# Kernel optimization log

Measured on AMD Instinct MI355X. Metric: run time of the kernel, lower is better.

## Reference

```python
import jax, jax.numpy as jnp
from jax import lax
import numpy as np

PAD_IDX = 4
KERNEL_SIZES = (2, 3, 4, 5)
N_FILTERS = 32
D_EMB = 8
D_OUT = 64
VOCAB = 5
B, L = 4096, 512
LN_EPS = 1e-5


def setup_inputs() -> dict:
    key = jax.random.key(0)
    ks = jax.random.split(key, 32)
    inp = {}
    inp['x_idx'] = jax.random.randint(ks[0], (B, L), 0, VOCAB, dtype=jnp.int64 if jax.config.jax_enable_x64 else jnp.int32)
    emb = jax.random.normal(ks[1], (VOCAB, D_EMB), dtype=jnp.float32) * 0.1
    inp['emb'] = emb.at[PAD_IDX].set(0.0)  # padding_idx row zero
    for i, kz in enumerate(KERNEL_SIZES):
        inp[f'conv_w{i}'] = jax.random.normal(ks[2 + 2 * i], (N_FILTERS, D_EMB, kz), dtype=jnp.float32) * (1.0 / np.sqrt(D_EMB * kz))
        inp[f'conv_b{i}'] = jnp.zeros((N_FILTERS,), jnp.float32)
        inp[f'att_w{i}'] = jax.random.normal(ks[3 + 2 * i], (N_FILTERS,), dtype=jnp.float32) * (1.0 / np.sqrt(N_FILTERS))
        inp[f'att_b{i}'] = jnp.zeros((1,), jnp.float32)
    inp['proj_w'] = jax.random.normal(ks[20], (D_OUT, N_FILTERS * len(KERNEL_SIZES)), dtype=jnp.float32) * (1.0 / np.sqrt(N_FILTERS * len(KERNEL_SIZES)))
    inp['proj_b'] = jnp.zeros((D_OUT,), jnp.float32)
    inp['gamma'] = jnp.ones((D_OUT,), jnp.float32)
    inp['beta'] = jnp.zeros((D_OUT,), jnp.float32)
    return inp


def _branch(X, W, b, aw, ab):
    # X: [B, C_in, L]; W: [C_out, C_in, ks]
    h = lax.conv_general_dilated(X, W, (1,), 'VALID',
                                 dimension_numbers=('NCH', 'OIH', 'NCH'))
    h = jax.nn.gelu(h + b[None, :, None], approximate=False)     # [B, F, L']
    scores = jnp.einsum('bfl,f->bl', h, aw) + ab[0]              # linear attn score
    w = jax.nn.softmax(scores, axis=1)                           # over positions
    return jnp.einsum('bfl,bl->bf', h, w)                        # weighted pool -> [B, F]


def reference(x_idx, emb, conv_w0, conv_b0, conv_w1, conv_b1, conv_w2, conv_b2,
              conv_w3, conv_b3, att_w0, att_b0, att_w1, att_b1, att_w2, att_b2,
              att_w3, att_b3, proj_w, proj_b, gamma, beta):
    emb = emb.at[PAD_IDX].set(0.0)
    X = emb[x_idx].transpose(0, 2, 1)  # [B, d_emb, L]
    feats = [
        _branch(X, conv_w0, conv_b0, att_w0, att_b0),
        _branch(X, conv_w1, conv_b1, att_w1, att_b1),
        _branch(X, conv_w2, conv_b2, att_w2, att_b2),
        _branch(X, conv_w3, conv_b3, att_w3, att_b3),
    ]
    z = jnp.concatenate(feats, axis=1)                 # [B, 4*F]
    z = z @ proj_w.T + proj_b                          # [B, D_OUT]
    z = jax.nn.gelu(z, approximate=False)
    mu = jnp.mean(z, axis=-1, keepdims=True)
    var = jnp.var(z, axis=-1, keepdims=True)
    return (z - mu) / jnp.sqrt(var + LN_EPS) * gamma + beta
```

## Files before the change

kernel.cpp:

```cpp
#include <hip/hip_runtime.h>
#include <math.h>

#define BATCH 4096
#define SEQL  512
#define NF    32
#define DEMB  8
#define DOUT  64

#define NWIN_TOTAL 3900
#define HWIN_OFF   4096

__device__ __forceinline__ float gelu_exact(float x) {
    return 0.5f * x * (1.0f + erff(x * 0.70710678118654752f));
}

__global__ __launch_bounds__(256) void precompute_tables(
    const float* __restrict__ emb,
    const float* __restrict__ cw0, const float* __restrict__ cb0,
    const float* __restrict__ aw0, const float* __restrict__ ab0,
    const float* __restrict__ cw1, const float* __restrict__ cb1,
    const float* __restrict__ aw1, const float* __restrict__ ab1,
    const float* __restrict__ cw2, const float* __restrict__ cb2,
    const float* __restrict__ aw2, const float* __restrict__ ab2,
    const float* __restrict__ cw3, const float* __restrict__ cb3,
    const float* __restrict__ aw3, const float* __restrict__ ab3,
    float* __restrict__ ws)
{
    const int gid = blockIdx.x * blockDim.x + threadIdx.x;
    if (gid >= NWIN_TOTAL * NF) return;
    const int wgid = gid >> 5;
    const int f    = gid & 31;

    int w, ks;
    const float *cw, *cb, *aw, *ab;
    if (wgid < 25)       { w = wgid;       ks = 2; cw = cw0; cb = cb0; aw = aw0; ab = ab0; }
    else if (wgid < 150) { w = wgid - 25;  ks = 3; cw = cw1; cb = cb1; aw = aw1; ab = ab1; }
    else if (wgid < 775) { w = wgid - 150; ks = 4; cw = cw2; cb = cb2; aw = aw2; ab = ab2; }
    else                 { w = wgid - 775; ks = 5; cw = cw3; cb = cb3; aw = aw3; ab = ab3; }

    float h = cb[f];
    int ww = w;
    for (int t = ks - 1; t >= 0; --t) {
        int d = ww % 5; ww /= 5;
        const float* e = emb + d * DEMB;
#pragma unroll
        for (int c = 0; c < DEMB; ++c)
            h += e[c] * cw[(f * DEMB + c) * ks + t];
    }
    float g = gelu_exact(h);
    ws[HWIN_OFF + wgid * NF + f] = g;

    float s = g * aw[f];
#pragma unroll
    for (int off = 16; off; off >>= 1) s += __shfl_xor(s, off, 32);
    if (f == 0) ws[wgid] = s + ab[0];
}

__global__ __launch_bounds__(256) void fused_main(
    const int*   __restrict__ xidx,
    const float* __restrict__ ws,
    const float* __restrict__ projw, const float* __restrict__ projb,
    const float* __restrict__ gamma, const float* __restrict__ beta,
    float* __restrict__ out)
{
    __shared__ int    xs[SEQL];
    __shared__ float2 pw[4][SEQL];
    __shared__ float  feat[4 * NF];

    const int b   = blockIdx.x;
    const int tid = threadIdx.x;

#pragma unroll
    for (int i = tid; i < SEQL / 4; i += 256)
        ((int4*)xs)[i] = ((const int4*)(xidx + b * SEQL))[i];
    __syncthreads();

    const int wave = tid >> 6;
    const int lane = tid & 63;

    constexpr int KS[4]  = {2, 3, 4, 5};
    constexpr int LP[4]  = {511, 510, 509, 508};
    constexpr int SWB[4] = {0, 25, 150, 775};

    const int ks = KS[wave];
    const int Lp = LP[wave];
    const float* swin = ws + SWB[wave];
    const float* hwin = ws + HWIN_OFF + SWB[wave] * NF;

    float sv[8];
    float m = -INFINITY;
#pragma unroll
    for (int it = 0; it < 8; ++it) {
        int l = lane + it * 64;
        int w = 0; float s = -INFINITY;
        if (l < Lp) {
            w = xs[l];
            for (int t = 1; t < ks; ++t) w = w * 5 + xs[l + t];
            s = swin[w];
        }
        pw[wave][l].y = __int_as_float(w * (NF * 4));
        sv[it] = s;
        m = fmaxf(m, s);
    }
#pragma unroll
    for (int off = 32; off; off >>= 1) m = fmaxf(m, __shfl_xor(m, off));

    float ssum = 0.0f;
#pragma unroll
    for (int it = 0; it < 8; ++it) {
        int l = lane + it * 64;
        float e = __expf(sv[it] - m);
        pw[wave][l].x = e;
        ssum += e;
    }
#pragma unroll
    for (int off = 32; off; off >>= 1) ssum += __shfl_xor(ssum, off);
    const float inv = 1.0f / ssum;

    const int quad = lane & 7;
    const int pg   = lane >> 3;

    float a0 = 0.f, a1 = 0.f, a2 = 0.f, a3 = 0.f;
#pragma unroll 16
    for (int it = 0; it < 64; ++it) {
        const int pos = it * 8 + pg;
        float2 t = pw[wave][pos];
        const float p = t.x;
        const char* rowp = (const char*)hwin + __float_as_int(t.y);
        float4 r = *(const float4*)(rowp + quad * 16);
        a0 += p * r.x; a1 += p * r.y; a2 += p * r.z; a3 += p * r.w;
    }

#pragma unroll
    for (int off = 8; off < 64; off <<= 1) {
        a0 += __shfl_xor(a0, off);
        a1 += __shfl_xor(a1, off);
        a2 += __shfl_xor(a2, off);
        a3 += __shfl_xor(a3, off);
    }
    if (lane < 8) {
        float* fp = feat + wave * NF + lane * 4;
        fp[0] = a0 * inv; fp[1] = a1 * inv; fp[2] = a2 * inv; fp[3] = a3 * inv;
    }
    __syncthreads();

    if (tid < DOUT) {
        float z = projb[tid];
        const float4* pwr = (const float4*)(projw + tid * (4 * NF));
#pragma unroll
        for (int q = 0; q < 32; ++q) {
            float4 wq = pwr[q];
            const float* fj = feat + q * 4;
            z += wq.x * fj[0] + wq.y * fj[1] + wq.z * fj[2] + wq.w * fj[3];
        }
        z = gelu_exact(z);

        float s1 = z, s2 = z * z;
#pragma unroll
        for (int off = 32; off; off >>= 1) {
            s1 += __shfl_xor(s1, off);
            s2 += __shfl_xor(s2, off);
        }
        const float mu  = s1 * (1.0f / 64.0f);
        const float var = s2 * (1.0f / 64.0f) - mu * mu;
        const float r   = rsqrtf(var + 1e-5f);
        out[b * DOUT + tid] = (z - mu) * r * gamma[tid] + beta[tid];
    }
}

extern "C" void kernel_launch(void* const* d_in, const int* in_sizes, int n_in,
                              void* d_out, int out_size, void* d_ws, size_t ws_size,
                              hipStream_t stream) {
    const int*   xidx = (const int*)d_in[0];
    const float* emb  = (const float*)d_in[1];
    const float* cw[4]; const float* cb[4]; const float* aw[4]; const float* ab[4];
    for (int i = 0; i < 4; ++i) {
        cw[i] = (const float*)d_in[2 + 4 * i];
        cb[i] = (const float*)d_in[3 + 4 * i];
        aw[i] = (const float*)d_in[4 + 4 * i];
        ab[i] = (const float*)d_in[5 + 4 * i];
    }
    const float* projw = (const float*)d_in[18];
    const float* projb = (const float*)d_in[19];
    const float* gm    = (const float*)d_in[20];
    const float* bt    = (const float*)d_in[21];
    float* ws  = (float*)d_ws;
    float* out = (float*)d_out;

    hipLaunchKernelGGL(precompute_tables, dim3((NWIN_TOTAL * NF + 255) / 256), dim3(256), 0, stream,
                       emb,
                       cw[0], cb[0], aw[0], ab[0],
                       cw[1], cb[1], aw[1], ab[1],
                       cw[2], cb[2], aw[2], ab[2],
                       cw[3], cb[3], aw[3], ab[3],
                       ws);

    hipLaunchKernelGGL(fused_main, dim3(BATCH), dim3(256), 0, stream,
                       xidx, ws, projw, projb, gm, bt, out);
}
```

Measured before the change: 163.2 us.

## Store window tables in fp16, stage small tables in LDS, split pooling across waves

The precomputed GELU window tables are now stored as fp16. The ks=2 and ks=3 tables are copied into shared memory per block, while the ks=4 and ks=5 tables are still read from global/L2 as half8 vectors. The pooling loop is restructured so each wave handles a quarter of the positions for all four branches, with normalized softmax weights in LDS and a cross-wave partial-sum reduction. This aims to cut gather bandwidth and improve load balance, at the cost of extra LDS, one more barrier and fp16 rounding of the conv activations.

```diff
diff --git a/kernel.cpp b/kernel.cpp
--- a/kernel.cpp
+++ b/kernel.cpp
@@ -1,5 +1,8 @@
 #include <hip/hip_runtime.h>
 #include <math.h>
+
+typedef _Float16 half_t;
+typedef _Float16 half8 __attribute__((ext_vector_type(8)));
 
 #define BATCH 4096
 #define SEQL  512
@@ -48,7 +51,7 @@
             h += e[c] * cw[(f * DEMB + c) * ks + t];
     }
     float g = gelu_exact(h);
-    ws[HWIN_OFF + wgid * NF + f] = g;
+    ((half_t*)(ws + HWIN_OFF))[wgid * NF + f] = (half_t)g;
 
     float s = g * aw[f];
 #pragma unroll
@@ -64,83 +67,115 @@
     float* __restrict__ out)
 {
     __shared__ int    xs[SEQL];
-    __shared__ float2 pw[4][SEQL];
+    __shared__ float  pwS[4][SEQL];
+    __shared__ int    poffS[4][SEQL];
+    __shared__ half_t tabS[150 * NF];
+    __shared__ float  partial[4][4][NF];
     __shared__ float  feat[4 * NF];
 
     const int b   = blockIdx.x;
     const int tid = threadIdx.x;
+    const half_t* hwin16 = (const half_t*)(ws + HWIN_OFF);
 
 #pragma unroll
     for (int i = tid; i < SEQL / 4; i += 256)
         ((int4*)xs)[i] = ((const int4*)(xidx + b * SEQL))[i];
+#pragma unroll
+    for (int i = tid; i < 600; i += 256)
+        ((float4*)tabS)[i] = ((const float4*)hwin16)[i];
     __syncthreads();
 
     const int wave = tid >> 6;
     const int lane = tid & 63;
 
     constexpr int KS[4]  = {2, 3, 4, 5};
-    constexpr int LP[4]  = {511, 510, 509, 508};
     constexpr int SWB[4] = {0, 25, 150, 775};
 
-    const int ks = KS[wave];
-    const int Lp = LP[wave];
-    const float* swin = ws + SWB[wave];
-    const float* hwin = ws + HWIN_OFF + SWB[wave] * NF;
-
-    float sv[8];
-    float m = -INFINITY;
-#pragma unroll
-    for (int it = 0; it < 8; ++it) {
-        int l = lane + it * 64;
-        int w = 0; float s = -INFINITY;
-        if (l < Lp) {
-            w = xs[l];
-            for (int t = 1; t < ks; ++t) w = w * 5 + xs[l + t];
-            s = swin[w];
-        }
-        pw[wave][l].y = __int_as_float(w * (NF * 4));
-        sv[it] = s;
-        m = fmaxf(m, s);
-    }
-#pragma unroll
-    for (int off = 32; off; off >>= 1) m = fmaxf(m, __shfl_xor(m, off));
-
-    float ssum = 0.0f;
-#pragma unroll
-    for (int it = 0; it < 8; ++it) {
-        int l = lane + it * 64;
-        float e = __expf(sv[it] - m);
-        pw[wave][l].x = e;
-        ssum += e;
-    }
-#pragma unroll
-    for (int off = 32; off; off >>= 1) ssum += __shfl_xor(ssum, off);
-    const float inv = 1.0f / ssum;
-
-    const int quad = lane & 7;
-    const int pg   = lane >> 3;
-
-    float a0 = 0.f, a1 = 0.f, a2 = 0.f, a3 = 0.f;
-#pragma unroll 16
-    for (int it = 0; it < 64; ++it) {
-        const int pos = it * 8 + pg;
-        float2 t = pw[wave][pos];
-        const float p = t.x;
-        const char* rowp = (const char*)hwin + __float_as_int(t.y);
-        float4 r = *(const float4*)(rowp + quad * 16);
-        a0 += p * r.x; a1 += p * r.y; a2 += p * r.z; a3 += p * r.w;
-    }
-
-#pragma unroll
-    for (int off = 8; off < 64; off <<= 1) {
-        a0 += __shfl_xor(a0, off);
-        a1 += __shfl_xor(a1, off);
-        a2 += __shfl_xor(a2, off);
-        a3 += __shfl_xor(a3, off);
-    }
-    if (lane < 8) {
-        float* fp = feat + wave * NF + lane * 4;
-        fp[0] = a0 * inv; fp[1] = a1 * inv; fp[2] = a2 * inv; fp[3] = a3 * inv;
+    {
+        const int ks = KS[wave];
+        const int Lp = SEQL + 1 - ks;
+        const float* swin = ws + SWB[wave];
+
+        float sv[8];
+        float m = -INFINITY;
+#pragma unroll
+        for (int it = 0; it < 8; ++it) {
+            int l = lane + it * 64;
+            int w = 0; float s = -INFINITY;
+            if (l < Lp) {
+                w = xs[l];
+                for (int t = 1; t < ks; ++t) w = w * 5 + xs[l + t];
+                s = swin[w];
+            }
+            poffS[wave][l] = w << 6;
+            sv[it] = s;
+            m = fmaxf(m, s);
+        }
+#pragma unroll
+        for (int off = 32; off; off >>= 1) m = fmaxf(m, __shfl_xor(m, off));
+
+        float ssum = 0.0f;
+#pragma unroll
+        for (int it = 0; it < 8; ++it) {
+            sv[it] = __expf(sv[it] - m);
+            ssum += sv[it];
+        }
+#pragma unroll
+        for (int off = 32; off; off >>= 1) ssum += __shfl_xor(ssum, off);
+        const float inv = 1.0f / ssum;
+#pragma unroll
+        for (int it = 0; it < 8; ++it)
+            pwS[wave][lane + it * 64] = sv[it] * inv;
+    }
+    __syncthreads();
+
+    const int pl = lane & 15;
+    const int fq = lane >> 4;
+
+    const half_t* gtab2 = hwin16 + SWB[2] * NF;
+    const half_t* gtab3 = hwin16 + SWB[3] * NF;
+
+    float acc[4][8];
+#pragma unroll
+    for (int c = 0; c < 4; ++c)
+#pragma unroll
+        for (int j = 0; j < 8; ++j) acc[c][j] = 0.0f;
+
+#pragma unroll
+    for (int c = 0; c < 4; ++c) {
+#pragma unroll
+        for (int it = 0; it < 8; ++it) {
+            const int pos = (wave << 7) + (it << 4) + pl;
+            const float p = pwS[c][pos];
+            const int  off = poffS[c][pos];
+            half8 r;
+            if (c == 0)      r = *(const half8*)((const char*)tabS + off + fq * 16);
+            else if (c == 1) r = *(const half8*)((const char*)(tabS + 25 * NF) + off + fq * 16);
+            else if (c == 2) r = *(const half8*)((const char*)gtab2 + off + fq * 16);
+            else             r = *(const half8*)((const char*)gtab3 + off + fq * 16);
+#pragma unroll
+            for (int j = 0; j < 8; ++j)
+                acc[c][j] += p * (float)r[j];
+        }
+    }
+
+#pragma unroll
+    for (int c = 0; c < 4; ++c)
+#pragma unroll
+        for (int j = 0; j < 8; ++j) {
+            float v = acc[c][j];
+            v += __shfl_xor(v, 1);
+            v += __shfl_xor(v, 2);
+            v += __shfl_xor(v, 4);
+            v += __shfl_xor(v, 8);
+            if (pl == 0) partial[wave][c][fq * 8 + j] = v;
+        }
+    __syncthreads();
+
+    if (tid < 128) {
+        const int c = tid >> 5, f = tid & 31;
+        feat[c * NF + f] = partial[0][c][f] + partial[1][c][f]
+                         + partial[2][c][f] + partial[3][c][f];
     }
     __syncthreads();
 
```

Measured after the change: 213.6 us. 1.31x slower.
